# Kernel tuning notes

Measured on AMD Instinct MI355X. Metric: run time of the kernel, lower is better.

Reference implementation:

```python
import jax, jax.numpy as jnp
import numpy as np

T, B, I, H, O = 512, 256, 64, 512, 1


def setup_inputs() -> dict:
    key = jax.random.key(0)
    ks = jax.random.split(key, 7)
    s = 1.0 / np.sqrt(H)  # PyTorch RNN default init range
    u = lambda k, shape: jax.random.uniform(k, shape, jnp.float32, -s, s)
    return {
        "X": jax.random.normal(ks[0], (T, B, I), jnp.float32),
        "weight_ih": u(ks[1], (3 * H, I)),   # rows ordered [reset, update, new] as in torch
        "weight_hh": u(ks[2], (3 * H, H)),
        "bias_ih": u(ks[3], (3 * H,)),
        "bias_hh": u(ks[4], (3 * H,)),
        "value_weight": u(ks[5], (O, H)),    # nn.Linear(hidden, output, bias=False)
        "bias": jnp.zeros((O,), jnp.float32),  # self.bias parameter, init 0
    }


def _gru_scan(X, weight_ih, weight_hh, bias_ih, bias_hh):
    """Single-layer GRU, time-major X: (T, B, I) -> hidden states Z: (T, B, H)."""
    hidden = weight_hh.shape[1]
    # Precompute all input projections in one big GEMM: (T, B, 3H)
    gi = jnp.einsum('tbi,gi->tbg', X, weight_ih) + bias_ih
    Whr, Whz, Whn = jnp.split(weight_hh, 3, axis=0)
    bhr, bhz, bhn = jnp.split(bias_hh, 3)

    def step(h, gi_t):
        gir, giz, gin = jnp.split(gi_t, 3, axis=-1)
        r = jax.nn.sigmoid(gir + h @ Whr.T + bhr)
        z = jax.nn.sigmoid(giz + h @ Whz.T + bhz)
        n = jnp.tanh(gin + r * (h @ Whn.T + bhn))
        h_new = (1.0 - z) * n + z * h
        return h_new, h_new

    h0 = jnp.zeros((X.shape[1], hidden), X.dtype)
    h_last, Z = jax.lax.scan(step, h0, gi)
    return Z, h_last


def reference(X, weight_ih, weight_hh, bias_ih, bias_hh, value_weight, bias):
    Z, h_last = _gru_scan(X, weight_ih, weight_hh, bias_ih, bias_hh)
    # V = self.bias + self.value(Z)
    V = bias + jnp.einsum('tbh,oh->tbo', Z, value_weight)
    return V
```

## Files before the change

### kernel.cpp

```cpp
#include <hip/hip_runtime.h>
#include <hip/hip_fp16.h>


#define T_  512
#define B_  256
#define I_  64
#define H_  512
#define NBG 16
#define BT  16
#define HS  32
#define BLOCK 192
#define NSL 32

typedef _Float16 f16;
typedef _Float16 f16x8 __attribute__((ext_vector_type(8)));
typedef float    f32x4 __attribute__((ext_vector_type(4)));
typedef unsigned int u32x2 __attribute__((ext_vector_type(2)));

__device__ __forceinline__ float sigmoid_f(float x) { return 1.f / (1.f + __expf(-x)); }
__device__ __forceinline__ float tanh_f(float x) {
    float e2 = __expf(2.f * x);
    return 1.f - 2.f / (e2 + 1.f);
}

__global__ __launch_bounds__(BLOCK, 1) void gru_persistent(
    const float* __restrict__ X, const float* __restrict__ Wih,
    const float* __restrict__ Whh, const float* __restrict__ bih,
    const float* __restrict__ bhh, const float* __restrict__ vw,
    const float* __restrict__ bias, float* __restrict__ Vout,
    f16* __restrict__ hbuf, unsigned int* __restrict__ flags,
    float* __restrict__ part, const int use_part)
{
    const int blk  = blockIdx.x;
    const int g    = (blk & 7) * 2 + (blk >> 7);
    const int j    = (blk >> 3) & 15;
    const int b0   = g * BT;
    const int tid  = threadIdx.x;
    const int wv   = tid >> 6;
    const int lane = tid & 63;
    const int quad = lane >> 4;
    const int mrow = lane & 15;

    __shared__ __align__(16) f16 sh_x[2][BT][I_ + 8];
    unsigned int* gflags = flags + (size_t)g * 32;

    if (wv < 2) {
        f16x8 wh[3][16];
        f16x8 wxA[3][2];
        const int um = HS * j + wv * 16 + mrow;
        #pragma unroll
        for (int g3 = 0; g3 < 3; g3++) {
            const size_t grow = (size_t)(g3 * H_ + um);
            #pragma unroll
            for (int kt = 0; kt < 16; kt++) {
                const float* src = Whh + grow * H_ + kt * 32 + quad * 8;
                #pragma unroll
                for (int e = 0; e < 8; e++) wh[g3][kt][e] = (f16)src[e];
            }
            #pragma unroll
            for (int kt = 0; kt < 2; kt++) {
                const float* src = Wih + grow * I_ + kt * 32 + quad * 8;
                #pragma unroll
                for (int e = 0; e < 8; e++) wxA[g3][kt][e] = (f16)src[e];
            }
        }
        float b_r4[4], b_z4[4], b_ni4[4], b_nh4[4], vw4[4];
        #pragma unroll
        for (int r = 0; r < 4; r++) {
            const int ub = HS * j + wv * 16 + quad * 4 + r;
            b_r4[r]  = bih[ub] + bhh[ub];
            b_z4[r]  = bih[H_ + ub] + bhh[H_ + ub];
            b_ni4[r] = bih[2 * H_ + ub];
            b_nh4[r] = bhh[2 * H_ + ub];
            vw4[r]   = vw[ub];
        }
        float hprev[4] = {0.f, 0.f, 0.f, 0.f};
        unsigned int* myflag = gflags + (j * 2 + wv);
        const int sl = j * 2 + wv;
        const float bias0 = bias[0];

        __syncthreads();

        #pragma unroll 1
        for (int t = 0; t < T_; t++) {
            if (t > 0) {
                const unsigned target = (unsigned)t;
                for (;;) {
                    unsigned v = target;
                    if (lane < 32) {
                        const unsigned int* fp = gflags + lane;
                        asm volatile("global_load_dword %0, %1, off sc0 sc1\n\t"
                                     "s_waitcnt vmcnt(0)"
                                     : "=v"(v) : "v"(fp) : "memory");
                    }
                    if (__ballot(v >= target) == ~0ull) break;
                }
            }

            f16x8 afr[16];
            const char* pb = (const char*)(hbuf
                           + ((size_t)((t & 1) ^ 1) * NBG + g) * 8192)
                           + quad * 256 + mrow * 16;
            asm volatile(
                "global_load_dwordx4 %0, %16, off sc0 sc1\n\t"
                "global_load_dwordx4 %1, %16, off offset:1024 sc0 sc1\n\t"
                "global_load_dwordx4 %2, %16, off offset:2048 sc0 sc1\n\t"
                "global_load_dwordx4 %3, %16, off offset:3072 sc0 sc1\n\t"
                "global_load_dwordx4 %4, %17, off sc0 sc1\n\t"
                "global_load_dwordx4 %5, %17, off offset:1024 sc0 sc1\n\t"
                "global_load_dwordx4 %6, %17, off offset:2048 sc0 sc1\n\t"
                "global_load_dwordx4 %7, %17, off offset:3072 sc0 sc1\n\t"
                "global_load_dwordx4 %8, %18, off sc0 sc1\n\t"
                "global_load_dwordx4 %9, %18, off offset:1024 sc0 sc1\n\t"
                "global_load_dwordx4 %10, %18, off offset:2048 sc0 sc1\n\t"
                "global_load_dwordx4 %11, %18, off offset:3072 sc0 sc1\n\t"
                "global_load_dwordx4 %12, %19, off sc0 sc1\n\t"
                "global_load_dwordx4 %13, %19, off offset:1024 sc0 sc1\n\t"
                "global_load_dwordx4 %14, %19, off offset:2048 sc0 sc1\n\t"
                "global_load_dwordx4 %15, %19, off offset:3072 sc0 sc1\n\t"
                "s_waitcnt vmcnt(0)"
                : "=&v"(afr[0]), "=&v"(afr[1]), "=&v"(afr[2]), "=&v"(afr[3]),
                  "=&v"(afr[4]), "=&v"(afr[5]), "=&v"(afr[6]), "=&v"(afr[7]),
                  "=&v"(afr[8]), "=&v"(afr[9]), "=&v"(afr[10]), "=&v"(afr[11]),
                  "=&v"(afr[12]), "=&v"(afr[13]), "=&v"(afr[14]), "=&v"(afr[15])
                : "v"(pb), "v"(pb + 4096), "v"(pb + 8192), "v"(pb + 12288)
                : "memory");

            f16x8 bx0 = *(const f16x8*)&sh_x[t & 1][mrow][quad * 8];
            f16x8 bx1 = *(const f16x8*)&sh_x[t & 1][mrow][32 + quad * 8];
            const f32x4 zero = {0.f, 0.f, 0.f, 0.f};
            f32x4 a_r  = __builtin_amdgcn_mfma_f32_16x16x32_f16(wxA[0][0], bx0, zero, 0, 0, 0);
            f32x4 a_z  = __builtin_amdgcn_mfma_f32_16x16x32_f16(wxA[1][0], bx0, zero, 0, 0, 0);
            f32x4 a_ni = __builtin_amdgcn_mfma_f32_16x16x32_f16(wxA[2][0], bx0, zero, 0, 0, 0);
            a_r  = __builtin_amdgcn_mfma_f32_16x16x32_f16(wxA[0][1], bx1, a_r,  0, 0, 0);
            a_z  = __builtin_amdgcn_mfma_f32_16x16x32_f16(wxA[1][1], bx1, a_z,  0, 0, 0);
            a_ni = __builtin_amdgcn_mfma_f32_16x16x32_f16(wxA[2][1], bx1, a_ni, 0, 0, 0);
            f32x4 a_nh = zero;
            #pragma unroll
            for (int kt = 0; kt < 16; kt++) {
                a_r  = __builtin_amdgcn_mfma_f32_16x16x32_f16(wh[0][kt], afr[kt], a_r,  0, 0, 0);
                a_z  = __builtin_amdgcn_mfma_f32_16x16x32_f16(wh[1][kt], afr[kt], a_z,  0, 0, 0);
                a_nh = __builtin_amdgcn_mfma_f32_16x16x32_f16(wh[2][kt], afr[kt], a_nh, 0, 0, 0);
            }

            float hn[4];
            union { f16 h[4]; u32x2 v; } pk;
            #pragma unroll
            for (int r = 0; r < 4; r++) {
                float rg = sigmoid_f(a_r[r] + b_r4[r]);
                float zg = sigmoid_f(a_z[r] + b_z4[r]);
                float ng = tanh_f(a_ni[r] + b_ni4[r] + rg * (a_nh[r] + b_nh4[r]));
                hn[r] = (1.f - zg) * ng + zg * hprev[r];
                hprev[r] = hn[r];
                pk.h[r] = (f16)hn[r];
            }
            {
                f16* hp = hbuf + ((size_t)(t & 1) * NBG + g) * 8192
                        + (size_t)((4 * j + 2 * wv + (quad >> 1)) * 128
                                   + mrow * 8 + (quad & 1) * 4);
                asm volatile("global_store_dwordx2 %0, %1, off sc0 sc1"
                             :: "v"(hp), "v"(pk.v) : "memory");
            }
            float s = hn[0] * vw4[0] + hn[1] * vw4[1] + hn[2] * vw4[2] + hn[3] * vw4[3];
            s += __shfl_xor(s, 16);
            s += __shfl_xor(s, 32);

            asm volatile("s_waitcnt vmcnt(0)" ::: "memory");
            if (lane == 0)
                __hip_atomic_store(myflag, (unsigned)(t + 1),
                                   __ATOMIC_RELAXED, __HIP_MEMORY_SCOPE_AGENT);
            if (quad == 0) {
                if (use_part) part[(size_t)sl * (T_ * B_) + (size_t)t * B_ + b0 + mrow] = s;
                else atomicAdd(&Vout[(size_t)t * B_ + b0 + mrow], s + (sl == 0 ? bias0 : 0.f));
            }
            __syncthreads();
        }
    } else {
        const int bb = lane >> 2, seg = (lane & 3) * 16;
        {
            const float* xs = X + (size_t)(b0 + bb) * I_ + seg;
            const float4 x0 = *(const float4*)(xs + 0),  x1 = *(const float4*)(xs + 4);
            const float4 x2 = *(const float4*)(xs + 8),  x3 = *(const float4*)(xs + 12);
            f16* dst = &sh_x[0][bb][seg];
            f16x8 p0 = {(f16)x0.x,(f16)x0.y,(f16)x0.z,(f16)x0.w,(f16)x1.x,(f16)x1.y,(f16)x1.z,(f16)x1.w};
            f16x8 p1 = {(f16)x2.x,(f16)x2.y,(f16)x2.z,(f16)x2.w,(f16)x3.x,(f16)x3.y,(f16)x3.z,(f16)x3.w};
            *(f16x8*)dst = p0; *(f16x8*)(dst + 8) = p1;
        }
        __syncthreads();
        #pragma unroll 1
        for (int t = 0; t < T_; t++) {
            if (t + 1 < T_) {
                const float* xs = X + (size_t)(t + 1) * (B_ * I_) + (size_t)(b0 + bb) * I_ + seg;
                const float4 x0 = *(const float4*)(xs + 0),  x1 = *(const float4*)(xs + 4);
                const float4 x2 = *(const float4*)(xs + 8),  x3 = *(const float4*)(xs + 12);
                f16* dst = &sh_x[(t + 1) & 1][bb][seg];
                f16x8 p0 = {(f16)x0.x,(f16)x0.y,(f16)x0.z,(f16)x0.w,(f16)x1.x,(f16)x1.y,(f16)x1.z,(f16)x1.w};
                f16x8 p1 = {(f16)x2.x,(f16)x2.y,(f16)x2.z,(f16)x2.w,(f16)x3.x,(f16)x3.y,(f16)x3.z,(f16)x3.w};
                *(f16x8*)dst = p0; *(f16x8*)(dst + 8) = p1;
            }
            __syncthreads();
        }
    }
}

__global__ __launch_bounds__(256) void value_reduce(
    const float* __restrict__ part, const float* __restrict__ bias,
    float* __restrict__ Vout)
{
    const int i = blockIdx.x * 256 + threadIdx.x;
    float s = bias[0];
    #pragma unroll
    for (int sl = 0; sl < NSL; sl++) s += part[(size_t)sl * (T_ * B_) + i];
    Vout[i] = s;
}

extern "C" void kernel_launch(void* const* d_in, const int* in_sizes, int n_in,
                              void* d_out, int out_size, void* d_ws, size_t ws_size,
                              hipStream_t stream) {
    const float* X    = (const float*)d_in[0];
    const float* Wih  = (const float*)d_in[1];
    const float* Whh  = (const float*)d_in[2];
    const float* bih  = (const float*)d_in[3];
    const float* bhh  = (const float*)d_in[4];
    const float* vw   = (const float*)d_in[5];
    const float* bias = (const float*)d_in[6];
    float* Vout = (float*)d_out;

    f16* hbuf = (f16*)d_ws;
    const size_t hbytes    = (size_t)2 * B_ * H_ * sizeof(f16);
    const size_t flagbytes = (size_t)NBG * 32 * sizeof(unsigned);
    unsigned int* flags = (unsigned int*)((char*)d_ws + hbytes);
    float* part = (float*)((char*)d_ws + hbytes + flagbytes);
    const size_t partbytes = (size_t)NSL * T_ * B_ * sizeof(float);
    const int use_part = (ws_size >= hbytes + flagbytes + partbytes) ? 1 : 0;

    hipMemsetAsync(d_ws, 0, hbytes + flagbytes, stream);
    if (!use_part)
        hipMemsetAsync(d_out, 0, (size_t)out_size * sizeof(float), stream);

    gru_persistent<<<256, BLOCK, 0, stream>>>(X, Wih, Whh, bih, bhh, vw, bias,
                                              Vout, hbuf, flags, part, use_part);
    if (use_part)
        value_reduce<<<(T_ * B_) / 256, 256, 0, stream>>>(part, bias, Vout);
}
```

Baseline: 1.410 ms.

## Split hidden-state loads across waves via LDS and drop the X loader wave

Each of the two compute waves now loads only its own half of the previous hidden state from global memory. The halves are exchanged through shared memory with one barrier per step, which cuts the per-wave global load volume on the critical recurrent path. The separate X-prefetch wave is removed: compute waves load X directly at the top of each step, issued before the flag spin so the load latency is hidden. The recurrent matmul is skipped at t=0 because h0 is zero, which lets the hidden-buffer memset be dropped. In exchange, every step now pays an intra-block barrier and LDS traffic.

```diff
diff --git a/kernel.cpp b/kernel.cpp
--- a/kernel.cpp
+++ b/kernel.cpp
@@ -9,7 +9,7 @@
 #define NBG 16
 #define BT  16
 #define HS  32
-#define BLOCK 192
+#define BLOCK 128
 #define NSL 32
 
 typedef _Float16 f16;
@@ -41,49 +41,56 @@
     const int quad = lane >> 4;
     const int mrow = lane & 15;
 
-    __shared__ __align__(16) f16 sh_x[2][BT][I_ + 8];
+    __shared__ __align__(16) f16 sh_h[16][512];
     unsigned int* gflags = flags + (size_t)g * 32;
 
-    if (wv < 2) {
-        f16x8 wh[3][16];
-        f16x8 wxA[3][2];
-        const int um = HS * j + wv * 16 + mrow;
-        #pragma unroll
-        for (int g3 = 0; g3 < 3; g3++) {
-            const size_t grow = (size_t)(g3 * H_ + um);
+    f16x8 wh[3][16];
+    f16x8 wxA[3][2];
+    const int um = HS * j + wv * 16 + mrow;
+    #pragma unroll
+    for (int g3 = 0; g3 < 3; g3++) {
+        const size_t grow = (size_t)(g3 * H_ + um);
+        #pragma unroll
+        for (int kt = 0; kt < 16; kt++) {
+            const float* src = Whh + grow * H_ + kt * 32 + quad * 8;
             #pragma unroll
-            for (int kt = 0; kt < 16; kt++) {
-                const float* src = Whh + grow * H_ + kt * 32 + quad * 8;
-                #pragma unroll
-                for (int e = 0; e < 8; e++) wh[g3][kt][e] = (f16)src[e];
-            }
+            for (int e = 0; e < 8; e++) wh[g3][kt][e] = (f16)src[e];
+        }
+        #pragma unroll
+        for (int kt = 0; kt < 2; kt++) {
+            const float* src = Wih + grow * I_ + kt * 32 + quad * 8;
             #pragma unroll
-            for (int kt = 0; kt < 2; kt++) {
-                const float* src = Wih + grow * I_ + kt * 32 + quad * 8;
-                #pragma unroll
-                for (int e = 0; e < 8; e++) wxA[g3][kt][e] = (f16)src[e];
-            }
-        }
-        float b_r4[4], b_z4[4], b_ni4[4], b_nh4[4], vw4[4];
-        #pragma unroll
-        for (int r = 0; r < 4; r++) {
-            const int ub = HS * j + wv * 16 + quad * 4 + r;
-            b_r4[r]  = bih[ub] + bhh[ub];
-            b_z4[r]  = bih[H_ + ub] + bhh[H_ + ub];
-            b_ni4[r] = bih[2 * H_ + ub];
-            b_nh4[r] = bhh[2 * H_ + ub];
-            vw4[r]   = vw[ub];
-        }
-        float hprev[4] = {0.f, 0.f, 0.f, 0.f};
-        unsigned int* myflag = gflags + (j * 2 + wv);
-        const int sl = j * 2 + wv;
-        const float bias0 = bias[0];
-
-        __syncthreads();
-
-        #pragma unroll 1
-        for (int t = 0; t < T_; t++) {
-            if (t > 0) {
+            for (int e = 0; e < 8; e++) wxA[g3][kt][e] = (f16)src[e];
+        }
+    }
+    float b_r4[4], b_z4[4], b_ni4[4], b_nh4[4], vw4[4];
+    #pragma unroll
+    for (int r = 0; r < 4; r++) {
+        const int ub = HS * j + wv * 16 + quad * 4 + r;
+        b_r4[r]  = bih[ub] + bhh[ub];
+        b_z4[r]  = bih[H_ + ub] + bhh[H_ + ub];
+        b_ni4[r] = bih[2 * H_ + ub];
+        b_nh4[r] = bhh[2 * H_ + ub];
+        vw4[r]   = vw[ub];
+    }
+    float hprev[4] = {0.f, 0.f, 0.f, 0.f};
+    unsigned int* myflag = gflags + (j * 2 + wv);
+    const int sl = j * 2 + wv;
+    const float bias0 = bias[0];
+
+    #pragma unroll 1
+    for (int t = 0; t < T_; t++) {
+        const float* xb = X + (size_t)t * (B_ * I_) + (size_t)(b0 + mrow) * I_ + quad * 8;
+        const f32x4 xv0 = *(const f32x4*)xb;
+        const f32x4 xv1 = *(const f32x4*)(xb + 4);
+        const f32x4 xv2 = *(const f32x4*)(xb + 32);
+        const f32x4 xv3 = *(const f32x4*)(xb + 36);
+
+        const f32x4 zero = {0.f, 0.f, 0.f, 0.f};
+        f32x4 a_r = zero, a_z = zero, a_nh = zero;
+
+        if (t > 0) {
+            {
                 const unsigned target = (unsigned)t;
                 for (;;) {
                     unsigned v = target;
@@ -97,108 +104,95 @@
                 }
             }
 
-            f16x8 afr[16];
+            f16x8 own[8];
             const char* pb = (const char*)(hbuf
                            + ((size_t)((t & 1) ^ 1) * NBG + g) * 8192)
-                           + quad * 256 + mrow * 16;
+                           + (size_t)wv * 8192 + quad * 256 + mrow * 16;
             asm volatile(
-                "global_load_dwordx4 %0, %16, off sc0 sc1\n\t"
-                "global_load_dwordx4 %1, %16, off offset:1024 sc0 sc1\n\t"
-                "global_load_dwordx4 %2, %16, off offset:2048 sc0 sc1\n\t"
-                "global_load_dwordx4 %3, %16, off offset:3072 sc0 sc1\n\t"
-                "global_load_dwordx4 %4, %17, off sc0 sc1\n\t"
-                "global_load_dwordx4 %5, %17, off offset:1024 sc0 sc1\n\t"
-                "global_load_dwordx4 %6, %17, off offset:2048 sc0 sc1\n\t"
-                "global_load_dwordx4 %7, %17, off offset:3072 sc0 sc1\n\t"
-                "global_load_dwordx4 %8, %18, off sc0 sc1\n\t"
-                "global_load_dwordx4 %9, %18, off offset:1024 sc0 sc1\n\t"
-                "global_load_dwordx4 %10, %18, off offset:2048 sc0 sc1\n\t"
-                "global_load_dwordx4 %11, %18, off offset:3072 sc0 sc1\n\t"
-                "global_load_dwordx4 %12, %19, off sc0 sc1\n\t"
-                "global_load_dwordx4 %13, %19, off offset:1024 sc0 sc1\n\t"
-                "global_load_dwordx4 %14, %19, off offset:2048 sc0 sc1\n\t"
-                "global_load_dwordx4 %15, %19, off offset:3072 sc0 sc1\n\t"
+                "global_load_dwordx4 %0, %8, off sc0 sc1\n\t"
+                "global_load_dwordx4 %1, %8, off offset:1024 sc0 sc1\n\t"
+                "global_load_dwordx4 %2, %8, off offset:2048 sc0 sc1\n\t"
+                "global_load_dwordx4 %3, %8, off offset:3072 sc0 sc1\n\t"
+                "global_load_dwordx4 %4, %9, off sc0 sc1\n\t"
+                "global_load_dwordx4 %5, %9, off offset:1024 sc0 sc1\n\t"
+                "global_load_dwordx4 %6, %9, off offset:2048 sc0 sc1\n\t"
+                "global_load_dwordx4 %7, %9, off offset:3072 sc0 sc1\n\t"
                 "s_waitcnt vmcnt(0)"
-                : "=&v"(afr[0]), "=&v"(afr[1]), "=&v"(afr[2]), "=&v"(afr[3]),
-                  "=&v"(afr[4]), "=&v"(afr[5]), "=&v"(afr[6]), "=&v"(afr[7]),
-                  "=&v"(afr[8]), "=&v"(afr[9]), "=&v"(afr[10]), "=&v"(afr[11]),
-                  "=&v"(afr[12]), "=&v"(afr[13]), "=&v"(afr[14]), "=&v"(afr[15])
-                : "v"(pb), "v"(pb + 4096), "v"(pb + 8192), "v"(pb + 12288)
+                : "=&v"(own[0]), "=&v"(own[1]), "=&v"(own[2]), "=&v"(own[3]),
+                  "=&v"(own[4]), "=&v"(own[5]), "=&v"(own[6]), "=&v"(own[7])
+                : "v"(pb), "v"(pb + 4096)
                 : "memory");
 
-            f16x8 bx0 = *(const f16x8*)&sh_x[t & 1][mrow][quad * 8];
-            f16x8 bx1 = *(const f16x8*)&sh_x[t & 1][mrow][32 + quad * 8];
-            const f32x4 zero = {0.f, 0.f, 0.f, 0.f};
-            f32x4 a_r  = __builtin_amdgcn_mfma_f32_16x16x32_f16(wxA[0][0], bx0, zero, 0, 0, 0);
-            f32x4 a_z  = __builtin_amdgcn_mfma_f32_16x16x32_f16(wxA[1][0], bx0, zero, 0, 0, 0);
-            f32x4 a_ni = __builtin_amdgcn_mfma_f32_16x16x32_f16(wxA[2][0], bx0, zero, 0, 0, 0);
-            a_r  = __builtin_amdgcn_mfma_f32_16x16x32_f16(wxA[0][1], bx1, a_r,  0, 0, 0);
-            a_z  = __builtin_amdgcn_mfma_f32_16x16x32_f16(wxA[1][1], bx1, a_z,  0, 0, 0);
-            a_ni = __builtin_amdgcn_mfma_f32_16x16x32_f16(wxA[2][1], bx1, a_ni, 0, 0, 0);
-            f32x4 a_nh = zero;
+            {
+                f16* dst = &sh_h[wv * 8][quad * 128 + mrow * 8];
+                #pragma unroll
+                for (int i = 0; i < 8; i++)
+                    *(f16x8*)(dst + i * 512) = own[i];
+            }
+            __syncthreads();
+
             #pragma unroll
-            for (int kt = 0; kt < 16; kt++) {
-                a_r  = __builtin_amdgcn_mfma_f32_16x16x32_f16(wh[0][kt], afr[kt], a_r,  0, 0, 0);
-                a_z  = __builtin_amdgcn_mfma_f32_16x16x32_f16(wh[1][kt], afr[kt], a_z,  0, 0, 0);
-                a_nh = __builtin_amdgcn_mfma_f32_16x16x32_f16(wh[2][kt], afr[kt], a_nh, 0, 0, 0);
-            }
-
-            float hn[4];
-            union { f16 h[4]; u32x2 v; } pk;
-            #pragma unroll
-            for (int r = 0; r < 4; r++) {
-                float rg = sigmoid_f(a_r[r] + b_r4[r]);
-                float zg = sigmoid_f(a_z[r] + b_z4[r]);
-                float ng = tanh_f(a_ni[r] + b_ni4[r] + rg * (a_nh[r] + b_nh4[r]));
-                hn[r] = (1.f - zg) * ng + zg * hprev[r];
-                hprev[r] = hn[r];
-                pk.h[r] = (f16)hn[r];
+            for (int i = 0; i < 8; i++) {
+                const int kt = wv * 8 + i;
+                a_r  = __builtin_amdgcn_mfma_f32_16x16x32_f16(wh[0][kt], own[i], a_r,  0, 0, 0);
+                a_z  = __builtin_amdgcn_mfma_f32_16x16x32_f16(wh[1][kt], own[i], a_z,  0, 0, 0);
+                a_nh = __builtin_amdgcn_mfma_f32_16x16x32_f16(wh[2][kt], own[i], a_nh, 0, 0, 0);
             }
             {
-                f16* hp = hbuf + ((size_t)(t & 1) * NBG + g) * 8192
-                        + (size_t)((4 * j + 2 * wv + (quad >> 1)) * 128
-                                   + mrow * 8 + (quad & 1) * 4);
-                asm volatile("global_store_dwordx2 %0, %1, off sc0 sc1"
-                             :: "v"(hp), "v"(pk.v) : "memory");
-            }
-            float s = hn[0] * vw4[0] + hn[1] * vw4[1] + hn[2] * vw4[2] + hn[3] * vw4[3];
-            s += __shfl_xor(s, 16);
-            s += __shfl_xor(s, 32);
-
-            asm volatile("s_waitcnt vmcnt(0)" ::: "memory");
-            if (lane == 0)
-                __hip_atomic_store(myflag, (unsigned)(t + 1),
-                                   __ATOMIC_RELAXED, __HIP_MEMORY_SCOPE_AGENT);
-            if (quad == 0) {
-                if (use_part) part[(size_t)sl * (T_ * B_) + (size_t)t * B_ + b0 + mrow] = s;
-                else atomicAdd(&Vout[(size_t)t * B_ + b0 + mrow], s + (sl == 0 ? bias0 : 0.f));
-            }
-            __syncthreads();
-        }
-    } else {
-        const int bb = lane >> 2, seg = (lane & 3) * 16;
+                const f16* src = &sh_h[(wv ^ 1) * 8][quad * 128 + mrow * 8];
+                #pragma unroll
+                for (int i = 0; i < 8; i++) {
+                    const int kt = (wv ^ 1) * 8 + i;
+                    const f16x8 hb = *(const f16x8*)(src + i * 512);
+                    a_r  = __builtin_amdgcn_mfma_f32_16x16x32_f16(wh[0][kt], hb, a_r,  0, 0, 0);
+                    a_z  = __builtin_amdgcn_mfma_f32_16x16x32_f16(wh[1][kt], hb, a_z,  0, 0, 0);
+                    a_nh = __builtin_amdgcn_mfma_f32_16x16x32_f16(wh[2][kt], hb, a_nh, 0, 0, 0);
+                }
+            }
+        }
+
+        f16x8 bx0, bx1;
+        #pragma unroll
+        for (int e = 0; e < 4; e++) {
+            bx0[e] = (f16)xv0[e]; bx0[4 + e] = (f16)xv1[e];
+            bx1[e] = (f16)xv2[e]; bx1[4 + e] = (f16)xv3[e];
+        }
+        f32x4 a_ni = __builtin_amdgcn_mfma_f32_16x16x32_f16(wxA[2][0], bx0, zero, 0, 0, 0);
+        a_ni = __builtin_amdgcn_mfma_f32_16x16x32_f16(wxA[2][1], bx1, a_ni, 0, 0, 0);
+        a_r  = __builtin_amdgcn_mfma_f32_16x16x32_f16(wxA[0][0], bx0, a_r,  0, 0, 0);
+        a_r  = __builtin_amdgcn_mfma_f32_16x16x32_f16(wxA[0][1], bx1, a_r,  0, 0, 0);
+        a_z  = __builtin_amdgcn_mfma_f32_16x16x32_f16(wxA[1][0], bx0, a_z,  0, 0, 0);
+        a_z  = __builtin_amdgcn_mfma_f32_16x16x32_f16(wxA[1][1], bx1, a_z,  0, 0, 0);
+
+        float hn[4];
+        union { f16 h[4]; u32x2 v; } pk;
+        #pragma unroll
+        for (int r = 0; r < 4; r++) {
+            float rg = sigmoid_f(a_r[r] + b_r4[r]);
+            float zg = sigmoid_f(a_z[r] + b_z4[r]);
+            float ng = tanh_f(a_ni[r] + b_ni4[r] + rg * (a_nh[r] + b_nh4[r]));
+            hn[r] = (1.f - zg) * ng + zg * hprev[r];
+            hprev[r] = hn[r];
+            pk.h[r] = (f16)hn[r];
+        }
         {
-            const float* xs = X + (size_t)(b0 + bb) * I_ + seg;
-            const float4 x0 = *(const float4*)(xs + 0),  x1 = *(const float4*)(xs + 4);
-            const float4 x2 = *(const float4*)(xs + 8),  x3 = *(const float4*)(xs + 12);
-            f16* dst = &sh_x[0][bb][seg];
-            f16x8 p0 = {(f16)x0.x,(f16)x0.y,(f16)x0.z,(f16)x0.w,(f16)x1.x,(f16)x1.y,(f16)x1.z,(f16)x1.w};
-            f16x8 p1 = {(f16)x2.x,(f16)x2.y,(f16)x2.z,(f16)x2.w,(f16)x3.x,(f16)x3.y,(f16)x3.z,(f16)x3.w};
-            *(f16x8*)dst = p0; *(f16x8*)(dst + 8) = p1;
-        }
-        __syncthreads();
-        #pragma unroll 1
-        for (int t = 0; t < T_; t++) {
-            if (t + 1 < T_) {
-                const float* xs = X + (size_t)(t + 1) * (B_ * I_) + (size_t)(b0 + bb) * I_ + seg;
-                const float4 x0 = *(const float4*)(xs + 0),  x1 = *(const float4*)(xs + 4);
-                const float4 x2 = *(const float4*)(xs + 8),  x3 = *(const float4*)(xs + 12);
-                f16* dst = &sh_x[(t + 1) & 1][bb][seg];
-                f16x8 p0 = {(f16)x0.x,(f16)x0.y,(f16)x0.z,(f16)x0.w,(f16)x1.x,(f16)x1.y,(f16)x1.z,(f16)x1.w};
-                f16x8 p1 = {(f16)x2.x,(f16)x2.y,(f16)x2.z,(f16)x2.w,(f16)x3.x,(f16)x3.y,(f16)x3.z,(f16)x3.w};
-                *(f16x8*)dst = p0; *(f16x8*)(dst + 8) = p1;
-            }
-            __syncthreads();
+            f16* hp = hbuf + ((size_t)(t & 1) * NBG + g) * 8192
+                    + (size_t)((4 * j + 2 * wv + (quad >> 1)) * 128
+                               + mrow * 8 + (quad & 1) * 4);
+            asm volatile("global_store_dwordx2 %0, %1, off sc0 sc1"
+                         :: "v"(hp), "v"(pk.v) : "memory");
+        }
+        float s = hn[0] * vw4[0] + hn[1] * vw4[1] + hn[2] * vw4[2] + hn[3] * vw4[3];
+        s += __shfl_xor(s, 16);
+        s += __shfl_xor(s, 32);
+
+        asm volatile("s_waitcnt vmcnt(0)" ::: "memory");
+        if (lane == 0)
+            __hip_atomic_store(myflag, (unsigned)(t + 1),
+                               __ATOMIC_RELAXED, __HIP_MEMORY_SCOPE_AGENT);
+        if (quad == 0) {
+            if (use_part) part[(size_t)sl * (T_ * B_) + (size_t)t * B_ + b0 + mrow] = s;
+            else atomicAdd(&Vout[(size_t)t * B_ + b0 + mrow], s + (sl == 0 ? bias0 : 0.f));
         }
     }
 }
@@ -234,7 +228,7 @@
     const size_t partbytes = (size_t)NSL * T_ * B_ * sizeof(float);
     const int use_part = (ws_size >= hbytes + flagbytes + partbytes) ? 1 : 0;
 
-    hipMemsetAsync(d_ws, 0, hbytes + flagbytes, stream);
+    hipMemsetAsync(flags, 0, flagbytes, stream);
     if (!use_part)
         hipMemsetAsync(d_out, 0, (size_t)out_size * sizeof(float), stream);
 
```

Measured after the change: 3.140 ms. 123% more time.
